# Kernel optimization log

Hardware: AMD Instinct MI355X
Metric: run time of the kernel (lower is better)

## Reference

```python
import jax, jax.numpy as jnp
import numpy as np

HID = 512
B, T, INP_DIM, ACT_DIM = 16, 1000, 4, 1
DT = 0.01  # t_const


def _masks(hid, dtype=jnp.float32):
    q, half, k = hid // 4, hid // 2, int(0.3 * hid)
    strthal = jnp.concatenate([jnp.zeros(q), jnp.ones(half), jnp.zeros(q), jnp.zeros(5 * hid)]).astype(dtype)
    tonic = jnp.concatenate([jnp.zeros(hid), jnp.ones(2 * hid), jnp.zeros(hid), jnp.ones(hid), jnp.zeros(hid)]).astype(dtype)
    alm_mask = jnp.concatenate([jnp.zeros(5 * hid), jnp.ones(hid)]).astype(dtype)
    alm2str_m = jnp.concatenate([jnp.ones((hid, hid - k)), jnp.zeros((hid, k))], axis=1).astype(dtype)
    thal2str_m = jnp.concatenate([jnp.zeros((q, hid)), jnp.ones((half, hid)), jnp.zeros((q, hid))], axis=0).astype(dtype)
    str2snr_m = jnp.concatenate([jnp.ones((hid, half)), jnp.zeros((hid, half))], axis=1).astype(dtype)
    str2gpe_m = jnp.concatenate([jnp.zeros((hid, half)), jnp.ones((hid, half))], axis=1).astype(dtype)
    alm_d = jnp.ones(hid, dtype).at[hid - k:].set(-1.0)  # diag of alm2alm_D
    return strthal, tonic, alm_mask, alm2str_m, thal2str_m, str2snr_m, str2gpe_m, alm_d


def _forward(inp, hn, x, inhib_stim, str2str_w, thal2alm_w, thal2str_w, alm2alm_w,
             alm2str_w, str2snr_w, str2gpe_w, gpe2stn_w, stn2snr_w, snr2thal_w,
             inp_weight, fc1, fc2, str2str_fixed):
    hid = str2str_w.shape[0]
    strthal, tonic, alm_mask, alm2str_m, thal2str_m, str2snr_m, str2gpe_m, alm_d = _masks(hid, inp.dtype)
    relu = jax.nn.relu
    # region-to-region effective weights (D matrices are (+/-) identity -> sign/col scale)
    str2str = -str2str_fixed              # str2str_mask is all zeros; D = -I
    alm2alm = relu(alm2alm_w) * alm_d[None, :]
    alm2str = alm2str_m * relu(alm2str_w)
    thal2alm = relu(thal2alm_w)
    thal2str = thal2str_m * relu(thal2str_w)
    str2snr = -(str2snr_m * relu(str2snr_w))
    str2gpe = -(str2gpe_m * relu(str2gpe_w))
    gpe2stn = -relu(gpe2stn_w)
    stn2snr = relu(stn2snr_w)
    snr2thal = -relu(snr2thal_w)
    H6 = 6 * hid
    W = jnp.zeros((H6, H6), inp.dtype)
    def blk(W, r, c, m):
        return W.at[r * hid:(r + 1) * hid, c * hid:(c + 1) * hid].set(m)
    # rows: str, gpe, stn, snr, thal, alm
    W = blk(W, 0, 0, str2str); W = blk(W, 0, 4, thal2str); W = blk(W, 0, 5, alm2str)
    W = blk(W, 1, 0, str2gpe)
    W = blk(W, 2, 1, gpe2stn)
    W = blk(W, 3, 0, str2snr); W = blk(W, 3, 2, stn2snr)
    W = blk(W, 4, 3, snr2thal)
    W = blk(W, 5, 4, thal2alm); W = blk(W, 5, 5, alm2alm)
    # precompute per-step external drive (noise=False path)
    drive = jnp.einsum('bti,ih->bth', inp, relu(inp_weight)) * strthal \
            + inhib_stim[:, None, :] + tonic  # [B,T,6h]
    def step(h, d_t):
        h_new = jax.nn.relu(h + DT * (-h + h @ W.T + d_t))
        return h_new, h_new
    h0 = hn[0]
    _, hs = jax.lax.scan(step, h0, jnp.swapaxes(drive, 0, 1))  # [T,B,6h]
    rnn_out = jnp.swapaxes(hs, 0, 1)                           # [B,T,6h]
    x_out = jnp.broadcast_to(x[0][:, None, :], rnn_out.shape)  # x is never updated
    hn_last = rnn_out[:, -1, :][None]
    x_last = x_out[:, -1, :][None]
    out = jax.nn.sigmoid((rnn_out * alm_mask) @ jax.nn.relu(fc1) @ jax.nn.relu(fc2))
    return out, hn_last, rnn_out, x_last, x_out


def setup_inputs() -> dict:
    key = jax.random.key(0)
    ks = jax.random.split(key, 17)
    u = lambda k, shape, hi: jax.random.uniform(k, shape, jnp.float32, 0.0, hi)
    hid = HID
    d = {
        'inp': jax.random.normal(ks[0], (B, T, INP_DIM), jnp.float32),
        'hn': jnp.zeros((1, B, 6 * hid), jnp.float32),
        'x': jnp.zeros((1, B, 6 * hid), jnp.float32),
        'inhib_stim': jnp.zeros((B, 6 * hid), jnp.float32),
        'str2str_w': u(ks[1], (hid, hid), 0.01),
        'thal2alm_w': u(ks[2], (hid, hid), 0.01),
        'thal2str_w': u(ks[3], (hid, hid), 0.01),
        'alm2alm_w': u(ks[4], (hid, hid), 0.01),
        'alm2str_w': u(ks[5], (hid, hid), 0.01),
        'str2snr_w': u(ks[6], (hid, hid), 0.01),
        'str2gpe_w': u(ks[7], (hid, hid), 0.01),
        'gpe2stn_w': u(ks[8], (hid, hid), 0.01),
        'stn2snr_w': u(ks[9], (hid, hid), 0.01),
        'snr2thal_w': u(ks[10], (hid, hid), 0.01),
        'inp_weight': u(ks[11], (INP_DIM, 6 * hid), 0.1),
        'fc1': u(ks[12], (6 * hid, hid), 0.01),
        'fc2': u(ks[13], (hid, ACT_DIM), 0.01),
    }
    sparse_mask = (jax.random.uniform(ks[14], (hid, hid)) < 0.1).astype(jnp.float32)
    d['str2str_fixed'] = u(ks[15], (hid, hid), 0.001) * sparse_mask
    return d


def reference(inp, hn, x, inhib_stim, str2str_w, thal2alm_w, thal2str_w, alm2alm_w,
              alm2str_w, str2snr_w, str2gpe_w, gpe2stn_w, stn2snr_w, snr2thal_w,
              inp_weight, fc1, fc2, str2str_fixed):
    return _forward(inp, hn, x, inhib_stim, str2str_w, thal2alm_w, thal2str_w,
                    alm2alm_w, alm2str_w, str2snr_w, str2gpe_w, gpe2stn_w,
                    stn2snr_w, snr2thal_w, inp_weight, fc1, fc2, str2str_fixed)
```

## Files before the change

kernel.cpp:

```cpp
#include <hip/hip_runtime.h>

#define H6   3072
#define TT   1000
#define NWG  192
#define NTHR 256

typedef short bf16x8 __attribute__((ext_vector_type(8)));
typedef float f32x4  __attribute__((ext_vector_type(4)));

#define TAG64 0x8000800080008000ull

__device__ __forceinline__ unsigned short f2bf(float f) {
  unsigned u = __float_as_uint(f);
  return (unsigned short)((u + 0x7fffu + ((u >> 16) & 1u)) >> 16);
}
__device__ __forceinline__ float bf2f(unsigned short s) {
  return __uint_as_float(((unsigned)s) << 16);
}

#define WS_WLO 5242880
#define WS_RHI 10485760
#define WS_RLO 11272192
#define WS_FCV 12058624


__global__ void prep_kernel(
    const float* __restrict__ hn, const float* __restrict__ fixed_,
    const float* __restrict__ thal2alm_w, const float* __restrict__ thal2str_w,
    const float* __restrict__ alm2alm_w, const float* __restrict__ alm2str_w,
    const float* __restrict__ str2snr_w, const float* __restrict__ str2gpe_w,
    const float* __restrict__ gpe2stn_w, const float* __restrict__ stn2snr_w,
    const float* __restrict__ snr2thal_w,
    const float* __restrict__ fc1, const float* __restrict__ fc2,
    unsigned short* __restrict__ Whi, unsigned short* __restrict__ Wlo,
    unsigned short* __restrict__ ringH, unsigned short* __restrict__ ringL,
    float* __restrict__ fc_vec)
{
  int gid = blockIdx.x * blockDim.x + threadIdx.x;
  int stride = gridDim.x * blockDim.x;
  const int nbt[6]  = {3,1,1,2,1,2};
  const int woff[6] = {0,786432,1048576,1310720,1835008,2097152};
  for (int idx = gid; idx < 2621440; idx += stride) {
    int u = idx >> 18;
    int t = (u<3)?0:((u<4)?1:((u<5)?2:((u<7)?3:((u<8)?4:5))));
    int local = idx - woff[t];
    int ktot = nbt[t] << 9;
    int j  = local / ktot;
    int kx = local - j*ktot;
    int bi = kx >> 9, kk = kx & 511;
    int src = j*512 + kk;
    float w;
    if (t == 0) {
      if (bi == 0)      w = -fixed_[src];
      else if (bi == 1) w = (j >= 128 && j < 384) ? fmaxf(thal2str_w[src],0.f) : 0.f;
      else              w = (kk < 359) ? fmaxf(alm2str_w[src],0.f) : 0.f;
    } else if (t == 1)  w = (kk >= 256) ? -fmaxf(str2gpe_w[src],0.f) : 0.f;
    else if (t == 2)    w = -fmaxf(gpe2stn_w[src],0.f);
    else if (t == 3)    w = (bi == 0) ? ((kk < 256) ? -fmaxf(str2snr_w[src],0.f) : 0.f)
                                      : fmaxf(stn2snr_w[src],0.f);
    else if (t == 4)    w = -fmaxf(snr2thal_w[src],0.f);
    else                w = (bi == 0) ? fmaxf(thal2alm_w[src],0.f)
                                      : fmaxf(alm2alm_w[src],0.f) * ((kk < 359) ? 1.f : -1.f);
    unsigned short hi = f2bf(w);
    Whi[idx] = hi;
    Wlo[idx] = f2bf(w - bf2f(hi));
  }
  for (int idx = gid; idx < 7*49152; idx += stride) {
    unsigned short pz = (idx & 1) ? 0x0000 : 0x8000;
    ringH[idx] = pz;
    ringL[idx] = pz;
  }
  for (int idx = gid; idx < 49152; idx += stride) {
    int region = idx >> 13;
    int rem    = idx & 8191;
    int q      = rem >> 9;
    int rem2   = rem & 511;
    int b      = rem2 >> 5;
    int jin    = rem2 & 31;
    int j      = (region << 9) + (q << 5) + jin;
    float v = hn[b * H6 + j];
    unsigned uh = __float_as_uint(v) >> 16;
    float lof = v - __uint_as_float(uh << 16);
    unsigned ul = __float_as_uint(lof) >> 16;
    ringH[7*49152 + idx] = (unsigned short)(uh | 0x8000u);
    ringL[7*49152 + idx] = (unsigned short)(ul | 0x8000u);
  }
  int wid = gid >> 6, lane = gid & 63;
  if (wid < 512) {
    float s = 0.f;
    for (int m = lane; m < 512; m += 64)
      s += fmaxf(fc1[(2560 + wid)*512 + m], 0.f) * fmaxf(fc2[m], 0.f);
    for (int off = 32; off; off >>= 1) s += __shfl_down(s, off);
    if (lane == 0) fc_vec[wid] = s;
  }
}

template<int NB>
__device__ __forceinline__ void scan_body(
    const float* __restrict__ inp, const float* __restrict__ hn,
    const float* __restrict__ inhib, const float* __restrict__ inp_weight,
    const unsigned short* __restrict__ Whi_g, const unsigned short* __restrict__ Wlo_g,
    unsigned short* __restrict__ ringH, unsigned short* __restrict__ ringL,
    float* __restrict__ rnn_out,
    float* red, int type, int tile, int kb0, int kb1, int kb2, int woff)
{
  constexpr int NCW = NB * 4;
  const int tid = threadIdx.x, lane = tid & 63, wave = tid >> 6;
  const int ktot = NB << 9;
  const int jb_local = tile << 4;
  const int jb_glob  = (type << 9) + jb_local;
  const int row = lane & 15, quad = lane >> 4;

  bf16x8 wh[NCW], wl[NCW];
  int hoff[NCW];
  {
    const unsigned short* sh = Whi_g + woff + (jb_local + row) * ktot + (quad << 3);
    const unsigned short* sl = Wlo_g + woff + (jb_local + row) * ktot + (quad << 3);
    #pragma unroll
    for (int c = 0; c < NCW; ++c) {
      int gc = wave * NCW + c;
      wh[c] = *(const bf16x8*)(sh + (gc << 5));
      wl[c] = *(const bf16x8*)(sl + (gc << 5));
      int bi = gc >> 4;
      int kbv = (bi == 0) ? kb0 : ((bi == 1) ? kb1 : kb2);
      hoff[c] = (kbv << 13) + ((gc & 15) << 9) + (row << 5) + (quad << 3);
    }
  }
  #pragma unroll
  for (int c = 0; c < NCW; ++c)
    asm volatile("" : "+v"(wh[c]), "+v"(wl[c]));

  const int b_ep = row;
  const bool has_inp = (type == 0) && (jb_local >= 128) && (jb_local < 384);
  const int jg0 = jb_glob + (quad << 2);
  const int jl0 = jb_local + (quad << 2);
  const int ring_st = (type << 13) + ((jl0 >> 5) << 9) + (b_ep << 5) + (jl0 & 31);
  float hprev[4], dbase[4], iw[4][4];
  #pragma unroll
  for (int r = 0; r < 4; ++r) {
    int jgr = jg0 + r;
    hprev[r] = hn[b_ep * H6 + jgr];
    float tn = ((jgr >= 512 && jgr < 1536) || (jgr >= 2048 && jgr < 2560)) ? 1.f : 0.f;
    dbase[r] = inhib[b_ep * H6 + jgr] + tn;
    #pragma unroll
    for (int i = 0; i < 4; ++i)
      iw[r][i] = has_inp ? fmaxf(inp_weight[i * H6 + jgr], 0.f) : 0.f;
  }

  for (int t = 0; t < TT; ++t) {
    const int s_rd = (t + 7) & 7;
    const unsigned short* gh = ringH + s_rd * 49152;
    const unsigned short* gl = ringL + s_rd * 49152;
    const unsigned long long exp = (((t - 1) >> 3) & 1) ? TAG64 : 0ull;

    float4 xi = {0.f, 0.f, 0.f, 0.f};
    if (wave == 0 && has_inp) xi = *(const float4*)(inp + (b_ep * TT + t) * 4);

    unsigned long long bh[NCW][2], bl[NCW][2];
    for (;;) {
      #pragma unroll
      for (int c = 0; c < NCW; ++c) {
        const unsigned long long* ph = (const unsigned long long*)(gh + hoff[c]);
        const unsigned long long* pl = (const unsigned long long*)(gl + hoff[c]);
        bh[c][0] = __hip_atomic_load(ph,     __ATOMIC_RELAXED, __HIP_MEMORY_SCOPE_AGENT);
        bh[c][1] = __hip_atomic_load(ph + 1, __ATOMIC_RELAXED, __HIP_MEMORY_SCOPE_AGENT);
        bl[c][0] = __hip_atomic_load(pl,     __ATOMIC_RELAXED, __HIP_MEMORY_SCOPE_AGENT);
        bl[c][1] = __hip_atomic_load(pl + 1, __ATOMIC_RELAXED, __HIP_MEMORY_SCOPE_AGENT);
      }
      unsigned long long bad = 0ull;
      #pragma unroll
      for (int c = 0; c < NCW; ++c)
        bad |= (bh[c][0] ^ exp) | (bh[c][1] ^ exp) | (bl[c][0] ^ exp) | (bl[c][1] ^ exp);
      if (__all((bad & TAG64) == 0ull)) break;
      __builtin_amdgcn_s_sleep(1);
    }
    #pragma unroll
    for (int c = 0; c < NCW; ++c) {
      bh[c][0] &= ~TAG64; bh[c][1] &= ~TAG64;
      bl[c][0] &= ~TAG64; bl[c][1] &= ~TAG64;
    }

    f32x4 acc0 = {0,0,0,0}, acc1 = {0,0,0,0}, acc2 = {0,0,0,0};
    #pragma unroll
    for (int c = 0; c < NCW; ++c) {
      bf16x8 hb, lb;
      ((unsigned long long*)&hb)[0] = bh[c][0];
      ((unsigned long long*)&hb)[1] = bh[c][1];
      ((unsigned long long*)&lb)[0] = bl[c][0];
      ((unsigned long long*)&lb)[1] = bl[c][1];
      acc0 = __builtin_amdgcn_mfma_f32_16x16x32_bf16(wh[c], hb, acc0, 0, 0, 0);
      acc1 = __builtin_amdgcn_mfma_f32_16x16x32_bf16(wh[c], lb, acc1, 0, 0, 0);
      acc2 = __builtin_amdgcn_mfma_f32_16x16x32_bf16(wl[c], hb, acc2, 0, 0, 0);
    }
    f32x4 acc = acc0 + acc1 + acc2;

    float* bank = red + (t & 1) * 768;
    if (wave) *(f32x4*)(bank + ((wave - 1) * 64 + lane) * 4) = acc;
    __syncthreads();
    if (wave == 0) {
      acc = acc + *(const f32x4*)(bank + lane * 4)
                + *(const f32x4*)(bank + (64 + lane) * 4)
                + *(const f32x4*)(bank + (128 + lane) * 4);
      float proj[4] = {0.f, 0.f, 0.f, 0.f};
      if (has_inp) {
        #pragma unroll
        for (int r = 0; r < 4; ++r)
          proj[r] = xi.x*iw[r][0] + xi.y*iw[r][1] + xi.z*iw[r][2] + xi.w*iw[r][3];
      }
      const unsigned long long ptag = ((t >> 3) & 1) ? TAG64 : 0ull;
      float4 hv4;
      unsigned long long ph = 0ull, pl = 0ull;
      #pragma unroll
      for (int r = 0; r < 4; ++r) {
        float pre = hprev[r] + 0.01f * (acc[r] + dbase[r] + proj[r] - hprev[r]);
        float hv = fmaxf(pre, 0.f);
        hprev[r] = hv;
        ((float*)&hv4)[r] = hv;
        unsigned uh = __float_as_uint(hv) >> 16;
        float lof = hv - __uint_as_float(uh << 16);
        unsigned ul = __float_as_uint(lof) >> 16;
        ph |= ((unsigned long long)uh) << (16 * r);
        pl |= ((unsigned long long)ul) << (16 * r);
      }
      ph |= ptag; pl |= ptag;
      unsigned long long* oh = (unsigned long long*)(ringH + (t & 7) * 49152 + ring_st);
      unsigned long long* ol = (unsigned long long*)(ringL + (t & 7) * 49152 + ring_st);
      __hip_atomic_store(oh, ph, __ATOMIC_RELAXED, __HIP_MEMORY_SCOPE_AGENT);
      __hip_atomic_store(ol, pl, __ATOMIC_RELAXED, __HIP_MEMORY_SCOPE_AGENT);
      *(float4*)(rnn_out + (size_t)(b_ep * TT + t) * H6 + jg0) = hv4;
    }
  }
}

__global__ void __launch_bounds__(NTHR, 1) scan_kernel(
    const float* __restrict__ inp, const float* __restrict__ hn,
    const float* __restrict__ inhib, const float* __restrict__ inp_weight,
    const unsigned short* __restrict__ Whi_g, const unsigned short* __restrict__ Wlo_g,
    unsigned short* __restrict__ ringH, unsigned short* __restrict__ ringL,
    float* __restrict__ rnn_out)
{
  __shared__ float red[2 * 768];
  int wg = blockIdx.x;
  int type = wg >> 5, tile = wg & 31;
  switch (type) {
    case 0: scan_body<3>(inp,hn,inhib,inp_weight,Whi_g,Wlo_g,ringH,ringL,rnn_out,red,0,tile,0,4,5,0);       break;
    case 1: scan_body<1>(inp,hn,inhib,inp_weight,Whi_g,Wlo_g,ringH,ringL,rnn_out,red,1,tile,0,0,0,786432);  break;
    case 2: scan_body<1>(inp,hn,inhib,inp_weight,Whi_g,Wlo_g,ringH,ringL,rnn_out,red,2,tile,1,0,0,1048576); break;
    case 3: scan_body<2>(inp,hn,inhib,inp_weight,Whi_g,Wlo_g,ringH,ringL,rnn_out,red,3,tile,0,2,0,1310720); break;
    case 4: scan_body<1>(inp,hn,inhib,inp_weight,Whi_g,Wlo_g,ringH,ringL,rnn_out,red,4,tile,3,0,0,1835008); break;
    default:scan_body<2>(inp,hn,inhib,inp_weight,Whi_g,Wlo_g,ringH,ringL,rnn_out,red,5,tile,4,5,0,2097152); break;
  }
}

__global__ void head_kernel(const float* __restrict__ rnn, const float* __restrict__ fc_vec,
                            float* __restrict__ out, float* __restrict__ hn_last)
{
  int lane = threadIdx.x & 63;
  if (blockIdx.x < 4000) {
    int wid = blockIdx.x * 4 + (threadIdx.x >> 6);
    int b = wid / 1000, t = wid - b * 1000;
    const float* rp = rnn + (size_t)(b * 1000 + t) * H6 + 2560 + lane * 8;
    float4 a0 = *(const float4*)rp, a1 = *(const float4*)(rp + 4);
    const float* vp = fc_vec + lane * 8;
    float4 v0 = *(const float4*)vp, v1 = *(const float4*)(vp + 4);
    float s = a0.x*v0.x + a0.y*v0.y + a0.z*v0.z + a0.w*v0.w
            + a1.x*v1.x + a1.y*v1.y + a1.z*v1.z + a1.w*v1.w;
    for (int off = 32; off; off >>= 1) s += __shfl_down(s, off);
    if (lane == 0) out[b * 1000 + t] = 1.f / (1.f + expf(-s));
  } else {
    int idx = (blockIdx.x - 4000) * NTHR + threadIdx.x;
    int b = idx / H6, j = idx - b * H6;
    hn_last[idx] = rnn[(size_t)(b * 1000 + 999) * H6 + j];
  }
}

__global__ void bcast_kernel(const float* __restrict__ x,
                             float* __restrict__ x_last, float* __restrict__ x_out)
{
  int gid = blockIdx.x * blockDim.x + threadIdx.x;
  int stride = gridDim.x * blockDim.x;
  for (int i = gid; i < 12288; i += stride)
    ((float4*)x_last)[i] = ((const float4*)x)[i];
  for (int i = gid; i < 12288000; i += stride) {
    int b = i / 768000;
    int r = i - b * 768000;
    int j4 = r % 768;
    ((float4*)x_out)[i] = ((const float4*)x)[b * 768 + j4];
  }
}

extern "C" void kernel_launch(void* const* d_in, const int* in_sizes, int n_in,
                              void* d_out, int out_size, void* d_ws, size_t ws_size,
                              hipStream_t stream) {
  (void)in_sizes; (void)n_in; (void)out_size; (void)ws_size;
  const float* inp        = (const float*)d_in[0];
  const float* hn         = (const float*)d_in[1];
  const float* x          = (const float*)d_in[2];
  const float* inhib      = (const float*)d_in[3];
  const float* thal2alm_w = (const float*)d_in[5];
  const float* thal2str_w = (const float*)d_in[6];
  const float* alm2alm_w  = (const float*)d_in[7];
  const float* alm2str_w  = (const float*)d_in[8];
  const float* str2snr_w  = (const float*)d_in[9];
  const float* str2gpe_w  = (const float*)d_in[10];
  const float* gpe2stn_w  = (const float*)d_in[11];
  const float* stn2snr_w  = (const float*)d_in[12];
  const float* snr2thal_w = (const float*)d_in[13];
  const float* inp_weight = (const float*)d_in[14];
  const float* fc1        = (const float*)d_in[15];
  const float* fc2        = (const float*)d_in[16];
  const float* fixed_     = (const float*)d_in[17];

  float* out_p   = (float*)d_out;
  float* hn_last = out_p + 16000;
  float* rnn     = hn_last + 49152;
  float* x_last  = rnn + 49152000;
  float* x_out   = x_last + 49152;

  char* ws = (char*)d_ws;
  unsigned short* Whi   = (unsigned short*)(ws);
  unsigned short* Wlo   = (unsigned short*)(ws + WS_WLO);
  unsigned short* ringH = (unsigned short*)(ws + WS_RHI);
  unsigned short* ringL = (unsigned short*)(ws + WS_RLO);
  float* fc_vec   = (float*)(ws + WS_FCV);

  prep_kernel<<<2048, NTHR, 0, stream>>>(hn, fixed_, thal2alm_w, thal2str_w, alm2alm_w,
      alm2str_w, str2snr_w, str2gpe_w, gpe2stn_w, stn2snr_w, snr2thal_w, fc1, fc2,
      Whi, Wlo, ringH, ringL, fc_vec);
  scan_kernel<<<NWG, NTHR, 0, stream>>>(inp, hn, inhib, inp_weight,
      Whi, Wlo, ringH, ringL, rnn);
  head_kernel<<<4192, NTHR, 0, stream>>>(rnn, fc_vec, out_p, hn_last);
  bcast_kernel<<<4096, NTHR, 0, stream>>>(x, x_last, x_out);
}
```

Before: 6.201 ms.

## Interleave hi/lo ring buffers and poll with selective dwordx4 reloads

Merges the separate hi and lo bf16 ring buffers into one interleaved layout, so each 32-byte chunk holds the hi and lo halves next to each other. Each chunk is then fetched with two adjacent dwordx4 loads through inline asm that bypasses the cache, instead of four 64-bit atomic loads. The spin-wait now tracks which chunks are still stale and reloads only those, aiming to cut polling traffic and latency on the per-step cross-workgroup handoff. In exchange it depends on the ordering semantics of the inline asm loads with sc0 sc1, and on the new offset arithmetic being correct.

```diff
diff --git a/kernel.cpp b/kernel.cpp
--- a/kernel.cpp
+++ b/kernel.cpp
@@ -7,6 +7,7 @@
 
 typedef short bf16x8 __attribute__((ext_vector_type(8)));
 typedef float f32x4  __attribute__((ext_vector_type(4)));
+typedef unsigned int u32x4 __attribute__((ext_vector_type(4)));
 
 #define TAG64 0x8000800080008000ull
 
@@ -19,8 +20,7 @@
 }
 
 #define WS_WLO 5242880
-#define WS_RHI 10485760
-#define WS_RLO 11272192
+#define WS_RING 10485760
 #define WS_FCV 12058624
 
 
@@ -33,8 +33,7 @@
     const float* __restrict__ snr2thal_w,
     const float* __restrict__ fc1, const float* __restrict__ fc2,
     unsigned short* __restrict__ Whi, unsigned short* __restrict__ Wlo,
-    unsigned short* __restrict__ ringH, unsigned short* __restrict__ ringL,
-    float* __restrict__ fc_vec)
+    unsigned short* __restrict__ ring, float* __restrict__ fc_vec)
 {
   int gid = blockIdx.x * blockDim.x + threadIdx.x;
   int stride = gridDim.x * blockDim.x;
@@ -65,25 +64,23 @@
     Whi[idx] = hi;
     Wlo[idx] = f2bf(w - bf2f(hi));
   }
-  for (int idx = gid; idx < 7*49152; idx += stride) {
-    unsigned short pz = (idx & 1) ? 0x0000 : 0x8000;
-    ringH[idx] = pz;
-    ringL[idx] = pz;
-  }
-  for (int idx = gid; idx < 49152; idx += stride) {
-    int region = idx >> 13;
-    int rem    = idx & 8191;
-    int q      = rem >> 9;
-    int rem2   = rem & 511;
-    int b      = rem2 >> 5;
-    int jin    = rem2 & 31;
-    int j      = (region << 9) + (q << 5) + jin;
-    float v = hn[b * H6 + j];
-    unsigned uh = __float_as_uint(v) >> 16;
-    float lof = v - __uint_as_float(uh << 16);
+  for (int u = gid; u < 7*98304; u += stride)
+    ring[u] = (u & 1) ? (unsigned short)0x0000 : (unsigned short)0x8000;
+  for (int v = gid; v < 49152; v += stride) {
+    int r    = v >> 13;
+    int rem  = v & 8191;
+    int q    = rem >> 9;
+    int rem2 = rem & 511;
+    int b    = rem2 >> 5;
+    int ko   = rem2 & 31;
+    int j    = (r << 9) + (q << 5) + ko;
+    float val = hn[b * H6 + j];
+    unsigned uh = __float_as_uint(val) >> 16;
+    float lof = val - __uint_as_float(uh << 16);
     unsigned ul = __float_as_uint(lof) >> 16;
-    ringH[7*49152 + idx] = (unsigned short)(uh | 0x8000u);
-    ringL[7*49152 + idx] = (unsigned short)(ul | 0x8000u);
+    int off = r*16384 + q*1024 + b*64 + ((ko>>3)<<4) + (ko & 7);
+    ring[7*98304 + off]     = (unsigned short)(uh | 0x8000u);
+    ring[7*98304 + off + 8] = (unsigned short)(ul | 0x8000u);
   }
   int wid = gid >> 6, lane = gid & 63;
   if (wid < 512) {
@@ -100,8 +97,7 @@
     const float* __restrict__ inp, const float* __restrict__ hn,
     const float* __restrict__ inhib, const float* __restrict__ inp_weight,
     const unsigned short* __restrict__ Whi_g, const unsigned short* __restrict__ Wlo_g,
-    unsigned short* __restrict__ ringH, unsigned short* __restrict__ ringL,
-    float* __restrict__ rnn_out,
+    unsigned short* __restrict__ ring, float* __restrict__ rnn_out,
     float* red, int type, int tile, int kb0, int kb1, int kb2, int woff)
 {
   constexpr int NCW = NB * 4;
@@ -112,7 +108,7 @@
   const int row = lane & 15, quad = lane >> 4;
 
   bf16x8 wh[NCW], wl[NCW];
-  int hoff[NCW];
+  int coff[NCW];
   {
     const unsigned short* sh = Whi_g + woff + (jb_local + row) * ktot + (quad << 3);
     const unsigned short* sl = Wlo_g + woff + (jb_local + row) * ktot + (quad << 3);
@@ -123,7 +119,7 @@
       wl[c] = *(const bf16x8*)(sl + (gc << 5));
       int bi = gc >> 4;
       int kbv = (bi == 0) ? kb0 : ((bi == 1) ? kb1 : kb2);
-      hoff[c] = (kbv << 13) + ((gc & 15) << 9) + (row << 5) + (quad << 3);
+      coff[c] = kbv*32768 + (gc & 15)*2048 + row*128 + quad*32;
     }
   }
   #pragma unroll
@@ -134,7 +130,8 @@
   const bool has_inp = (type == 0) && (jb_local >= 128) && (jb_local < 384);
   const int jg0 = jb_glob + (quad << 2);
   const int jl0 = jb_local + (quad << 2);
-  const int ring_st = (type << 13) + ((jl0 >> 5) << 9) + (b_ep << 5) + (jl0 & 31);
+  const int qs = jl0 >> 5, kos = jl0 & 31;
+  const int st_off = type*32768 + qs*2048 + b_ep*128 + ((kos>>3)<<5) + ((kos&7)<<1);
   float hprev[4], dbase[4], iw[4][4];
   #pragma unroll
   for (int r = 0; r < 4; ++r) {
@@ -149,45 +146,48 @@
 
   for (int t = 0; t < TT; ++t) {
     const int s_rd = (t + 7) & 7;
-    const unsigned short* gh = ringH + s_rd * 49152;
-    const unsigned short* gl = ringL + s_rd * 49152;
-    const unsigned long long exp = (((t - 1) >> 3) & 1) ? TAG64 : 0ull;
+    const char* slotp = (const char*)ring + s_rd * 196608;
+    const unsigned e32 = ((((t - 1) >> 3) & 1) ? 0x80008000u : 0u);
 
     float4 xi = {0.f, 0.f, 0.f, 0.f};
     if (wave == 0 && has_inp) xi = *(const float4*)(inp + (b_ep * TT + t) * 4);
 
-    unsigned long long bh[NCW][2], bl[NCW][2];
+    u32x4 Bhi[NCW], Blo[NCW];
+    unsigned todo = (NCW == 12) ? 0xFFFu : ((NCW == 8) ? 0xFFu : 0xFu);
     for (;;) {
       #pragma unroll
-      for (int c = 0; c < NCW; ++c) {
-        const unsigned long long* ph = (const unsigned long long*)(gh + hoff[c]);
-        const unsigned long long* pl = (const unsigned long long*)(gl + hoff[c]);
-        bh[c][0] = __hip_atomic_load(ph,     __ATOMIC_RELAXED, __HIP_MEMORY_SCOPE_AGENT);
-        bh[c][1] = __hip_atomic_load(ph + 1, __ATOMIC_RELAXED, __HIP_MEMORY_SCOPE_AGENT);
-        bl[c][0] = __hip_atomic_load(pl,     __ATOMIC_RELAXED, __HIP_MEMORY_SCOPE_AGENT);
-        bl[c][1] = __hip_atomic_load(pl + 1, __ATOMIC_RELAXED, __HIP_MEMORY_SCOPE_AGENT);
+      for (int c = 0; c < NCW; ++c) if ((todo >> c) & 1u) {
+        const char* pc = slotp + coff[c];
+        asm volatile("global_load_dwordx4 %0, %2, off sc0 sc1\n\t"
+                     "global_load_dwordx4 %1, %2, off offset:16 sc0 sc1"
+                     : "=&v"(Bhi[c]), "=&v"(Blo[c]) : "v"(pc) : "memory");
       }
-      unsigned long long bad = 0ull;
+      asm volatile("s_waitcnt vmcnt(0)" ::: "memory");
+      __builtin_amdgcn_sched_barrier(0);
+      unsigned nt = 0;
       #pragma unroll
-      for (int c = 0; c < NCW; ++c)
-        bad |= (bh[c][0] ^ exp) | (bh[c][1] ^ exp) | (bl[c][0] ^ exp) | (bl[c][1] ^ exp);
-      if (__all((bad & TAG64) == 0ull)) break;
+      for (int c = 0; c < NCW; ++c) if ((todo >> c) & 1u) {
+        unsigned bad = ((Bhi[c][0] ^ e32) | (Bhi[c][1] ^ e32) |
+                        (Bhi[c][2] ^ e32) | (Bhi[c][3] ^ e32) |
+                        (Blo[c][0] ^ e32) | (Blo[c][1] ^ e32) |
+                        (Blo[c][2] ^ e32) | (Blo[c][3] ^ e32)) & 0x80008000u;
+        if (__any(bad != 0u)) nt |= 1u << c;
+      }
+      if (nt == 0) break;
+      todo = nt;
       __builtin_amdgcn_s_sleep(1);
     }
     #pragma unroll
     for (int c = 0; c < NCW; ++c) {
-      bh[c][0] &= ~TAG64; bh[c][1] &= ~TAG64;
-      bl[c][0] &= ~TAG64; bl[c][1] &= ~TAG64;
+      Bhi[c] &= 0x7fff7fffu;
+      Blo[c] &= 0x7fff7fffu;
     }
 
     f32x4 acc0 = {0,0,0,0}, acc1 = {0,0,0,0}, acc2 = {0,0,0,0};
     #pragma unroll
     for (int c = 0; c < NCW; ++c) {
-      bf16x8 hb, lb;
-      ((unsigned long long*)&hb)[0] = bh[c][0];
-      ((unsigned long long*)&hb)[1] = bh[c][1];
-      ((unsigned long long*)&lb)[0] = bl[c][0];
-      ((unsigned long long*)&lb)[1] = bl[c][1];
+      bf16x8 hb = __builtin_bit_cast(bf16x8, Bhi[c]);
+      bf16x8 lb = __builtin_bit_cast(bf16x8, Blo[c]);
       acc0 = __builtin_amdgcn_mfma_f32_16x16x32_bf16(wh[c], hb, acc0, 0, 0, 0);
       acc1 = __builtin_amdgcn_mfma_f32_16x16x32_bf16(wh[c], lb, acc1, 0, 0, 0);
       acc2 = __builtin_amdgcn_mfma_f32_16x16x32_bf16(wl[c], hb, acc2, 0, 0, 0);
@@ -223,10 +223,11 @@
         pl |= ((unsigned long long)ul) << (16 * r);
       }
       ph |= ptag; pl |= ptag;
-      unsigned long long* oh = (unsigned long long*)(ringH + (t & 7) * 49152 + ring_st);
-      unsigned long long* ol = (unsigned long long*)(ringL + (t & 7) * 49152 + ring_st);
-      __hip_atomic_store(oh, ph, __ATOMIC_RELAXED, __HIP_MEMORY_SCOPE_AGENT);
-      __hip_atomic_store(ol, pl, __ATOMIC_RELAXED, __HIP_MEMORY_SCOPE_AGENT);
+      char* outb = (char*)ring + (t & 7) * 196608 + st_off;
+      __hip_atomic_store((unsigned long long*)outb, ph,
+                         __ATOMIC_RELAXED, __HIP_MEMORY_SCOPE_AGENT);
+      __hip_atomic_store((unsigned long long*)(outb + 16), pl,
+                         __ATOMIC_RELAXED, __HIP_MEMORY_SCOPE_AGENT);
       *(float4*)(rnn_out + (size_t)(b_ep * TT + t) * H6 + jg0) = hv4;
     }
   }
@@ -236,19 +237,18 @@
     const float* __restrict__ inp, const float* __restrict__ hn,
     const float* __restrict__ inhib, const float* __restrict__ inp_weight,
     const unsigned short* __restrict__ Whi_g, const unsigned short* __restrict__ Wlo_g,
-    unsigned short* __restrict__ ringH, unsigned short* __restrict__ ringL,
-    float* __restrict__ rnn_out)
+    unsigned short* __restrict__ ring, float* __restrict__ rnn_out)
 {
   __shared__ float red[2 * 768];
   int wg = blockIdx.x;
   int type = wg >> 5, tile = wg & 31;
   switch (type) {
-    case 0: scan_body<3>(inp,hn,inhib,inp_weight,Whi_g,Wlo_g,ringH,ringL,rnn_out,red,0,tile,0,4,5,0);       break;
-    case 1: scan_body<1>(inp,hn,inhib,inp_weight,Whi_g,Wlo_g,ringH,ringL,rnn_out,red,1,tile,0,0,0,786432);  break;
-    case 2: scan_body<1>(inp,hn,inhib,inp_weight,Whi_g,Wlo_g,ringH,ringL,rnn_out,red,2,tile,1,0,0,1048576); break;
-    case 3: scan_body<2>(inp,hn,inhib,inp_weight,Whi_g,Wlo_g,ringH,ringL,rnn_out,red,3,tile,0,2,0,1310720); break;
-    case 4: scan_body<1>(inp,hn,inhib,inp_weight,Whi_g,Wlo_g,ringH,ringL,rnn_out,red,4,tile,3,0,0,1835008); break;
-    default:scan_body<2>(inp,hn,inhib,inp_weight,Whi_g,Wlo_g,ringH,ringL,rnn_out,red,5,tile,4,5,0,2097152); break;
+    case 0: scan_body<3>(inp,hn,inhib,inp_weight,Whi_g,Wlo_g,ring,rnn_out,red,0,tile,0,4,5,0);       break;
+    case 1: scan_body<1>(inp,hn,inhib,inp_weight,Whi_g,Wlo_g,ring,rnn_out,red,1,tile,0,0,0,786432);  break;
+    case 2: scan_body<1>(inp,hn,inhib,inp_weight,Whi_g,Wlo_g,ring,rnn_out,red,2,tile,1,0,0,1048576); break;
+    case 3: scan_body<2>(inp,hn,inhib,inp_weight,Whi_g,Wlo_g,ring,rnn_out,red,3,tile,0,2,0,1310720); break;
+    case 4: scan_body<1>(inp,hn,inhib,inp_weight,Whi_g,Wlo_g,ring,rnn_out,red,4,tile,3,0,0,1835008); break;
+    default:scan_body<2>(inp,hn,inhib,inp_weight,Whi_g,Wlo_g,ring,rnn_out,red,5,tile,4,5,0,2097152); break;
   }
 }
 
@@ -318,17 +318,16 @@
   float* x_out   = x_last + 49152;
 
   char* ws = (char*)d_ws;
-  unsigned short* Whi   = (unsigned short*)(ws);
-  unsigned short* Wlo   = (unsigned short*)(ws + WS_WLO);
-  unsigned short* ringH = (unsigned short*)(ws + WS_RHI);
-  unsigned short* ringL = (unsigned short*)(ws + WS_RLO);
-  float* fc_vec   = (float*)(ws + WS_FCV);
+  unsigned short* Whi  = (unsigned short*)(ws);
+  unsigned short* Wlo  = (unsigned short*)(ws + WS_WLO);
+  unsigned short* ring = (unsigned short*)(ws + WS_RING);
+  float* fc_vec  = (float*)(ws + WS_FCV);
 
   prep_kernel<<<2048, NTHR, 0, stream>>>(hn, fixed_, thal2alm_w, thal2str_w, alm2alm_w,
       alm2str_w, str2snr_w, str2gpe_w, gpe2stn_w, stn2snr_w, snr2thal_w, fc1, fc2,
-      Whi, Wlo, ringH, ringL, fc_vec);
+      Whi, Wlo, ring, fc_vec);
   scan_kernel<<<NWG, NTHR, 0, stream>>>(inp, hn, inhib, inp_weight,
-      Whi, Wlo, ringH, ringL, rnn);
+      Whi, Wlo, ring, rnn);
   head_kernel<<<4192, NTHR, 0, stream>>>(rnn, fc_vec, out_p, hn_last);
   bcast_kernel<<<4096, NTHR, 0, stream>>>(x, x_last, x_out);
 }
```

Result: faster. 5.986 ms (-3.5%).
